# Performance work log

Hardware: AMD Instinct MI355X
Metric: run time of the kernel (lower is better)

The kernel has to match this reference:

```python
import jax, jax.numpy as jnp
import numpy as np

N_EMBD = 768
N_HEADS = 12
HEAD_DIM = N_EMBD // N_HEADS


def _layernorm(x):
    # LayerNorm without affine params, eps=1e-5 (torch default)
    mu = jnp.mean(x, axis=-1, keepdims=True)
    var = jnp.var(x, axis=-1, keepdims=True)
    return (x - mu) * jax.lax.rsqrt(var + 1e-5)


def setup_inputs() -> dict:
    key = jax.random.key(0)
    ks = jax.random.split(key, 6)
    B, T, C = 1, 4096, N_EMBD
    s = lambda fan_in: 1.0 / np.sqrt(fan_in)
    return {
        "x": jax.random.normal(ks[0], (B, T, C), jnp.float32),
        "W_kqv": jax.random.normal(ks[1], (C, 3 * C), jnp.float32) * s(C),
        "W_proj": jax.random.normal(ks[2], (C, C), jnp.float32) * s(C),
        "W_fc": jax.random.normal(ks[3], (C, 2 * C), jnp.float32) * s(C),
        "b_fc": jax.random.normal(ks[4], (2 * C,), jnp.float32) * s(C),
        "W_cproj": jax.random.normal(ks[5], (2 * C, C), jnp.float32) * s(2 * C),
    }


def _attention(h, W_kqv, W_proj):
    B, T, C = h.shape
    kqv = h @ W_kqv                       # (B, T, 3C)
    kqv = kqv.reshape(B, T, 3, N_HEADS, HEAD_DIM)
    k = kqv[:, :, 0]                      # (B, T, H, Dh) -- note k first, per source
    q = kqv[:, :, 1]
    v = kqv[:, :, 2]
    scale = HEAD_DIM ** -0.5
    scores = jnp.einsum('bqhd,bkhd->bhqk', q, k) * scale
    attn = jax.nn.softmax(scores, axis=-1)
    out = jnp.einsum('bhqk,bkhd->bqhd', attn, v).reshape(B, T, C)
    return out @ W_proj


def _mlp(h, W_fc, b_fc, W_cproj):
    h = h @ W_fc + b_fc
    h = jax.nn.gelu(h, approximate=False)  # torch nn.GELU default = exact erf
    return h @ W_cproj


def reference(x, W_kqv, W_proj, W_fc, b_fc, W_cproj):
    x = x + _attention(_layernorm(x), W_kqv, W_proj)
    x = x + _mlp(_layernorm(x), W_fc, b_fc, W_cproj)
    return x
```

## Files before the change

### kernel.cpp

```cpp
#include <hip/hip_runtime.h>
#include <hip/hip_bf16.h>
#include <math.h>

#define T_SEQ 4096
#define C_EMB 768
#define NHEAD 12
#define HDIM  64
#define NZ    4

typedef __bf16 bf16;
typedef __bf16 bf16x8 __attribute__((ext_vector_type(8)));
typedef __bf16 bf16x4 __attribute__((ext_vector_type(4)));
typedef float  f32x4  __attribute__((ext_vector_type(4)));
typedef float  f32x16 __attribute__((ext_vector_type(16)));


__device__ __forceinline__ void stage16(const void* g, void* ldsbase) {
  __builtin_amdgcn_global_load_lds(
      (__attribute__((address_space(1))) const unsigned int*)g,
      (__attribute__((address_space(3))) unsigned int*)ldsbase, 16, 0, 0);
}

__device__ __forceinline__ f32x16 zero16() {
  f32x16 z;
#pragma unroll
  for (int i = 0; i < 16; i++) z[i] = 0.f;
  return z;
}

__global__ void wt_transpose(const float* __restrict__ W, bf16* __restrict__ Wt,
                             int K, int N) {
  __shared__ float tile[32][33];
  const int n0 = blockIdx.x * 32, k0 = blockIdx.y * 32;
  const int tx = threadIdx.x & 31, ty = threadIdx.x >> 5;
#pragma unroll
  for (int i = 0; i < 32; i += 8)
    tile[ty + i][tx] = W[(size_t)(k0 + ty + i) * N + n0 + tx];
  __syncthreads();
#pragma unroll
  for (int i = 0; i < 32; i += 8)
    Wt[(size_t)(n0 + ty + i) * K + k0 + tx] = (bf16)tile[tx][ty + i];
}

__global__ void ln_rows(const float* __restrict__ x, bf16* __restrict__ y) {
  const int row = blockIdx.x;
  const float* xr = x + (size_t)row * C_EMB;
  const int t = threadIdx.x;
  float v0 = xr[t], v1 = xr[t + 256], v2 = xr[t + 512];
  float s  = v0 + v1 + v2;
  float ss = v0 * v0 + v1 * v1 + v2 * v2;
#pragma unroll
  for (int m = 1; m < 64; m <<= 1) {
    s += __shfl_xor(s, m);
    ss += __shfl_xor(ss, m);
  }
  __shared__ float bs[4], bq[4];
  const int w = t >> 6;
  if ((t & 63) == 0) { bs[w] = s; bq[w] = ss; }
  __syncthreads();
  s  = bs[0] + bs[1] + bs[2] + bs[3];
  ss = bq[0] + bq[1] + bq[2] + bq[3];
  const float mu  = s * (1.0f / C_EMB);
  const float var = ss * (1.0f / C_EMB) - mu * mu;
  const float rs  = rsqrtf(var + 1e-5f);
  bf16* yr = y + (size_t)row * C_EMB;
  yr[t]       = (bf16)((v0 - mu) * rs);
  yr[t + 256] = (bf16)((v1 - mu) * rs);
  yr[t + 512] = (bf16)((v2 - mu) * rs);
}

template <int EPI, int BN>
__global__ void gemm_bt(const bf16* __restrict__ A, const bf16* __restrict__ BT,
                        void* __restrict__ Cout, const float* __restrict__ res,
                        const float* __restrict__ bias, int M, int N, int K) {
  __shared__ __align__(16) bf16 As[128 * 64];
  __shared__ __align__(16) bf16 Bs[BN * 64];
  const int row0 = blockIdx.x * 128, col0 = blockIdx.y * BN;
  const int tid = threadIdx.x;
  const int w = tid >> 6, lane = tid & 63;
  const int wr = w >> 1, wc = w & 1;
  const int l15 = lane & 15, l4 = lane >> 4;
  constexpr int NF = BN / 32;

  f32x4 acc[4][NF];
#pragma unroll
  for (int m = 0; m < 4; m++)
#pragma unroll
    for (int n = 0; n < NF; n++) acc[m][n] = (f32x4){0.f, 0.f, 0.f, 0.f};

  const int rr = lane >> 3;
  const int c8 = (lane & 7) * 8;

  for (int k0 = 0; k0 < K; k0 += 64) {
    const bf16* gA = A + (size_t)(row0 + w * 32 + rr) * K + k0 + c8;
    const bf16* gB = BT + (size_t)(col0 + w * (BN / 4) + rr) * K + k0 + c8;
#pragma unroll
    for (int i = 0; i < 4; i++)
      stage16(gA + (size_t)(8 * i) * K, As + (w * 32 + 8 * i) * 64);
#pragma unroll
    for (int i = 0; i < BN / 32; i++)
      stage16(gB + (size_t)(8 * i) * K, Bs + (w * (BN / 4) + 8 * i) * 64);
    __syncthreads();

#pragma unroll
    for (int hh = 0; hh < 2; hh++) {
      bf16x8 af[4], bfv[NF];
#pragma unroll
      for (int m = 0; m < 4; m++)
        af[m] = *reinterpret_cast<const bf16x8*>(
            As + (wr * 64 + m * 16 + l15) * 64 + hh * 32 + l4 * 8);
#pragma unroll
      for (int n = 0; n < NF; n++)
        bfv[n] = *reinterpret_cast<const bf16x8*>(
            Bs + (wc * (BN / 2) + n * 16 + l15) * 64 + hh * 32 + l4 * 8);
#pragma unroll
      for (int m = 0; m < 4; m++)
#pragma unroll
        for (int n = 0; n < NF; n++)
          acc[m][n] = __builtin_amdgcn_mfma_f32_16x16x32_bf16(af[m], bfv[n], acc[m][n], 0, 0, 0);
    }
    __syncthreads();
  }

  const int orow = row0 + wr * 64;
  const int ocol = col0 + wc * (BN / 2);
#pragma unroll
  for (int m = 0; m < 4; m++) {
#pragma unroll
    for (int n = 0; n < NF; n++) {
      const int c = ocol + n * 16 + l15;
#pragma unroll
      for (int j = 0; j < 4; j++) {
        const int r = orow + m * 16 + l4 * 4 + j;
        const size_t idx = (size_t)r * N + c;
        const float v = acc[m][n][j];
        if (EPI == 0) {
          ((bf16*)Cout)[idx] = (bf16)v;
        } else if (EPI == 1) {
          ((float*)Cout)[idx] = res[idx] + v;
        } else if (EPI == 2) {
          const float h = v + bias[c];
          ((bf16*)Cout)[idx] = (bf16)(0.5f * h * (1.0f + erff(h * 0.70710678118f)));
        } else {
          ((float*)Cout)[idx] = res[idx] + v;
        }
      }
    }
  }
}

__global__ __launch_bounds__(256, 3)
void attn_fused(const bf16* __restrict__ kqv,
                bf16* __restrict__ Opart,
                float* __restrict__ Lpart) {
  const int qb = blockIdx.x, h = blockIdx.y, z = blockIdx.z;
  const int tid = threadIdx.x, w = tid >> 6, lane = tid & 63;
  const int l31 = lane & 31, hi = lane >> 5;

  __shared__ __align__(16) char KsB[128 * 144];
  __shared__ __align__(16) char VtB[64 * 272];

  const int qrow = qb * 128 + w * 32 + l31;
  const bf16* qp = kqv + (size_t)qrow * 2304 + 768 + h * 64;
  bf16x8 qf[4];
#pragma unroll
  for (int m = 0; m < 4; m++)
    qf[m] = *reinterpret_cast<const bf16x8*>(qp + hi * 8 + 16 * m);
  const float cscale = 0.125f * 1.4426950408889634f;
#pragma unroll
  for (int m = 0; m < 4; m++)
#pragma unroll
    for (int e = 0; e < 8; e++) qf[m][e] = (bf16)((float)qf[m][e] * cscale);

  bf16x8 ones;
#pragma unroll
  for (int e = 0; e < 8; e++) ones[e] = (bf16)1.0f;

  f32x16 accO0 = zero16(), accO1 = zero16(), accL = zero16();

  const int krow = tid >> 1;
  const int kc0 = (tid & 1) * 4;
  const int kb = tid & 31, db = tid >> 5;
  const int lb = ((kb >> 3) & 3) * 32 + ((kb >> 2) & 1) * 16 + (kb & 1) * 8 +
                 ((kb >> 1) & 1) * 4;

  const int kt0 = z * 8;

  bf16x8 kreg[4], vreg[4];
#define LOADKV(kt)                                                               \
  {                                                                              \
    const bf16* kp =                                                             \
        kqv + (size_t)((kt)*128 + krow) * 2304 + h * 64 + kc0 * 8;               \
    _Pragma("unroll") for (int i = 0; i < 4; i++)                                \
        kreg[i] = *reinterpret_cast<const bf16x8*>(kp + i * 8);                  \
    const bf16* vp =                                                             \
        kqv + (size_t)((kt)*128 + kb * 4) * 2304 + 1536 + h * 64 + db * 8;       \
    _Pragma("unroll") for (int r = 0; r < 4; r++)                                \
        vreg[r] = *reinterpret_cast<const bf16x8*>(vp + (size_t)r * 2304);       \
  }

  LOADKV(kt0);

  for (int kt = 0; kt < 8; kt++) {
    __syncthreads();
    {
      char* kdst = KsB + krow * 144;
#pragma unroll
      for (int i = 0; i < 4; i++)
        *reinterpret_cast<bf16x8*>(kdst + (kc0 + i) * 16) = kreg[i];
#pragma unroll
      for (int e = 0; e < 8; e++) {
        const int d = db * 8 + e;
        const bf16x4 pk4 = (bf16x4){vreg[0][e], vreg[1][e], vreg[2][e], vreg[3][e]};
        *reinterpret_cast<bf16x4*>(VtB + d * 272 + lb * 2) = pk4;
      }
    }
    __syncthreads();
    if (kt + 1 < 8) LOADKV(kt0 + kt + 1);

    bf16x8 pb[8];
#pragma unroll
    for (int t = 0; t < 4; t++) {
      f32x16 st = zero16();
#pragma unroll
      for (int m = 0; m < 4; m++) {
        const bf16x8 kf = *reinterpret_cast<const bf16x8*>(
            KsB + (size_t)(32 * t + l31) * 144 + (2 * m + hi) * 16);
        st = __builtin_amdgcn_mfma_f32_32x32x16_bf16(kf, qf[m], st, 0, 0, 0);
      }
#pragma unroll
      for (int reg = 0; reg < 16; reg++) {
        const float pv = exp2f(st[reg]);
        pb[2 * t + (reg >> 3)][(reg & 3) + 4 * ((reg >> 2) & 1)] = (bf16)pv;
      }
    }

#pragma unroll
    for (int mk = 0; mk < 8; mk++) {
      const bf16x8 vf0 = *reinterpret_cast<const bf16x8*>(
          VtB + (size_t)l31 * 272 + (2 * mk + hi) * 16);
      accO0 = __builtin_amdgcn_mfma_f32_32x32x16_bf16(vf0, pb[mk], accO0, 0, 0, 0);
      const bf16x8 vf1 = *reinterpret_cast<const bf16x8*>(
          VtB + (size_t)(32 + l31) * 272 + (2 * mk + hi) * 16);
      accO1 = __builtin_amdgcn_mfma_f32_32x32x16_bf16(vf1, pb[mk], accO1, 0, 0, 0);
      accL = __builtin_amdgcn_mfma_f32_32x32x16_bf16(ones, pb[mk], accL, 0, 0, 0);
    }
  }
#undef LOADKV

  bf16* Oq = Opart + (size_t)z * T_SEQ * C_EMB + (size_t)qrow * C_EMB + h * 64;
#pragma unroll
  for (int s4 = 0; s4 < 4; s4++) {
    const bf16x4 o0 = (bf16x4){(bf16)accO0[4 * s4 + 0], (bf16)accO0[4 * s4 + 1],
                               (bf16)accO0[4 * s4 + 2], (bf16)accO0[4 * s4 + 3]};
    *reinterpret_cast<bf16x4*>(Oq + 8 * s4 + 4 * hi) = o0;
    const bf16x4 o1 = (bf16x4){(bf16)accO1[4 * s4 + 0], (bf16)accO1[4 * s4 + 1],
                               (bf16)accO1[4 * s4 + 2], (bf16)accO1[4 * s4 + 3]};
    *reinterpret_cast<bf16x4*>(Oq + 32 + 8 * s4 + 4 * hi) = o1;
  }
  if (hi == 0)
    Lpart[(size_t)z * NHEAD * T_SEQ + (size_t)h * T_SEQ + qrow] = accL[0];
}

__global__ void attn_combine(const bf16* __restrict__ Opart,
                             const float* __restrict__ Lpart,
                             bf16* __restrict__ out) {
  const int q = blockIdx.x, t = threadIdx.x;
#pragma unroll
  for (int i = 0; i < 3; i++) {
    const int c = t + i * 256;
    const int h = c >> 6;
    float L = 0.f, O = 0.f;
#pragma unroll
    for (int z = 0; z < NZ; z++) {
      L += Lpart[(size_t)z * NHEAD * T_SEQ + (size_t)h * T_SEQ + q];
      O += (float)Opart[(size_t)z * T_SEQ * C_EMB + (size_t)q * C_EMB + c];
    }
    out[(size_t)q * C_EMB + c] = (bf16)(O / L);
  }
}

extern "C" void kernel_launch(void* const* d_in, const int* in_sizes, int n_in,
                              void* d_out, int out_size, void* d_ws, size_t ws_size,
                              hipStream_t stream) {
  const float* x       = (const float*)d_in[0];
  const float* W_kqv   = (const float*)d_in[1];
  const float* W_proj  = (const float*)d_in[2];
  const float* W_fc    = (const float*)d_in[3];
  const float* b_fc    = (const float*)d_in[4];
  const float* W_cproj = (const float*)d_in[5];
  float* outp = (float*)d_out;

  char* p = (char*)d_ws;
  bf16* Wkqv_t  = (bf16*)p; p += (size_t)2304 * 768 * 2;
  bf16* Wproj_t = (bf16*)p; p += (size_t)768 * 768 * 2;
  bf16* Wfc_t   = (bf16*)p; p += (size_t)1536 * 768 * 2;
  bf16* Wcp_t   = (bf16*)p; p += (size_t)768 * 1536 * 2;
  bf16* A1      = (bf16*)p; p += (size_t)4096 * 768 * 2;
  bf16* KQV     = (bf16*)p; p += (size_t)4096 * 2304 * 2;
  float* x1     = (float*)p; p += (size_t)4096 * 768 * 4;
  bf16* Opart   = (bf16*)p; p += (size_t)NZ * 4096 * 768 * 2;
  float* Lpart  = (float*)p; p += (size_t)NZ * NHEAD * 4096 * 4;
  bf16* attn_o = A1;
  bf16* A2     = KQV;
  bf16* Hg     = KQV + (size_t)4096 * 768;

  wt_transpose<<<dim3(2304 / 32, 768 / 32), 256, 0, stream>>>(W_kqv, Wkqv_t, 768, 2304);
  wt_transpose<<<dim3(768 / 32, 768 / 32), 256, 0, stream>>>(W_proj, Wproj_t, 768, 768);
  wt_transpose<<<dim3(1536 / 32, 768 / 32), 256, 0, stream>>>(W_fc, Wfc_t, 768, 1536);
  wt_transpose<<<dim3(768 / 32, 1536 / 32), 256, 0, stream>>>(W_cproj, Wcp_t, 1536, 768);

  ln_rows<<<4096, 256, 0, stream>>>(x, A1);
  gemm_bt<0, 128><<<dim3(32, 18), 256, 0, stream>>>(A1, Wkqv_t, KQV, nullptr, nullptr,
                                                    4096, 2304, 768);
  attn_fused<<<dim3(32, 12, NZ), 256, 0, stream>>>(KQV, Opart, Lpart);
  attn_combine<<<4096, 256, 0, stream>>>(Opart, Lpart, attn_o);
  gemm_bt<1, 64><<<dim3(32, 12), 256, 0, stream>>>(attn_o, Wproj_t, x1, x, nullptr,
                                                   4096, 768, 768);
  ln_rows<<<4096, 256, 0, stream>>>(x1, A2);
  gemm_bt<2, 64><<<dim3(32, 24), 256, 0, stream>>>(A2, Wfc_t, Hg, nullptr, b_fc,
                                                   4096, 1536, 768);
  gemm_bt<3, 64><<<dim3(32, 12), 256, 0, stream>>>(Hg, Wcp_t, outp, x1, nullptr,
                                                   4096, 768, 1536);
}
```

Baseline: 212.8 us.

## Fuse weight transposes and first layernorm into one prep kernel; remap attention grid

Combines the four weight-transpose launches and the first layernorm into a single prep kernel that dispatches on block index, cutting launch overhead and the idle tails between small kernels. The QKV GEMM moves from BN=128 to BN=64 to get more blocks. The attention grid is flattened to 1D with a swizzled mapping from block to (q-block, head, split), probably aimed at XCD/L2 locality. The softmax exp switches to the hardware exp2 builtin with a vectorized pack. The exp builtin may lose a little accuracy, and the smaller GEMM tile lowers data reuse per block.

```diff
diff --git a/kernel.cpp b/kernel.cpp
--- a/kernel.cpp
+++ b/kernel.cpp
@@ -14,6 +14,12 @@
 typedef float  f32x4  __attribute__((ext_vector_type(4)));
 typedef float  f32x16 __attribute__((ext_vector_type(16)));
 
+#if __has_builtin(__builtin_amdgcn_exp2f)
+#define EXP2 __builtin_amdgcn_exp2f
+#else
+#define EXP2 exp2f
+#endif
+
 
 __device__ __forceinline__ void stage16(const void* g, void* ldsbase) {
   __builtin_amdgcn_global_load_lds(
@@ -28,11 +34,12 @@
   return z;
 }
 
-__global__ void wt_transpose(const float* __restrict__ W, bf16* __restrict__ Wt,
-                             int K, int N) {
-  __shared__ float tile[32][33];
-  const int n0 = blockIdx.x * 32, k0 = blockIdx.y * 32;
-  const int tx = threadIdx.x & 31, ty = threadIdx.x >> 5;
+__device__ __forceinline__ void do_transpose(const float* __restrict__ W,
+                                             bf16* __restrict__ Wt, int K, int N,
+                                             int bx, int by, int tid,
+                                             float (*tile)[33]) {
+  const int n0 = bx * 32, k0 = by * 32;
+  const int tx = tid & 31, ty = tid >> 5;
 #pragma unroll
   for (int i = 0; i < 32; i += 8)
     tile[ty + i][tx] = W[(size_t)(k0 + ty + i) * N + n0 + tx];
@@ -42,10 +49,10 @@
     Wt[(size_t)(n0 + ty + i) * K + k0 + tx] = (bf16)tile[tx][ty + i];
 }
 
-__global__ void ln_rows(const float* __restrict__ x, bf16* __restrict__ y) {
-  const int row = blockIdx.x;
+__device__ __forceinline__ void do_ln(const float* __restrict__ x,
+                                      bf16* __restrict__ y, int row, int t,
+                                      float* red) {
   const float* xr = x + (size_t)row * C_EMB;
-  const int t = threadIdx.x;
   float v0 = xr[t], v1 = xr[t + 256], v2 = xr[t + 512];
   float s  = v0 + v1 + v2;
   float ss = v0 * v0 + v1 * v1 + v2 * v2;
@@ -54,12 +61,11 @@
     s += __shfl_xor(s, m);
     ss += __shfl_xor(ss, m);
   }
-  __shared__ float bs[4], bq[4];
   const int w = t >> 6;
-  if ((t & 63) == 0) { bs[w] = s; bq[w] = ss; }
+  if ((t & 63) == 0) { red[w] = s; red[4 + w] = ss; }
   __syncthreads();
-  s  = bs[0] + bs[1] + bs[2] + bs[3];
-  ss = bq[0] + bq[1] + bq[2] + bq[3];
+  s  = red[0] + red[1] + red[2] + red[3];
+  ss = red[4] + red[5] + red[6] + red[7];
   const float mu  = s * (1.0f / C_EMB);
   const float var = ss * (1.0f / C_EMB) - mu * mu;
   const float rs  = rsqrtf(var + 1e-5f);
@@ -67,6 +73,34 @@
   yr[t]       = (bf16)((v0 - mu) * rs);
   yr[t + 256] = (bf16)((v1 - mu) * rs);
   yr[t + 512] = (bf16)((v2 - mu) * rs);
+}
+
+__global__ void prep(const float* __restrict__ x, bf16* __restrict__ ln_out,
+                     const float* __restrict__ W_kqv, bf16* __restrict__ Wkqv_t,
+                     const float* __restrict__ W_proj, bf16* __restrict__ Wproj_t,
+                     const float* __restrict__ W_fc, bf16* __restrict__ Wfc_t,
+                     const float* __restrict__ W_cproj, bf16* __restrict__ Wcp_t) {
+  __shared__ float tile[32][33];
+  const int b = blockIdx.x, t = threadIdx.x;
+  if (b < 1728) {
+    do_transpose(W_kqv, Wkqv_t, 768, 2304, b % 72, b / 72, t, tile);
+  } else if (b < 2304) {
+    const int bb = b - 1728;
+    do_transpose(W_proj, Wproj_t, 768, 768, bb % 24, bb / 24, t, tile);
+  } else if (b < 3456) {
+    const int bb = b - 2304;
+    do_transpose(W_fc, Wfc_t, 768, 1536, bb % 48, bb / 48, t, tile);
+  } else if (b < 4608) {
+    const int bb = b - 3456;
+    do_transpose(W_cproj, Wcp_t, 1536, 768, bb % 24, bb / 24, t, tile);
+  } else {
+    do_ln(x, ln_out, b - 4608, t, &tile[0][0]);
+  }
+}
+
+__global__ void ln_rows(const float* __restrict__ x, bf16* __restrict__ y) {
+  __shared__ float red[8];
+  do_ln(x, y, blockIdx.x, threadIdx.x, red);
 }
 
 template <int EPI, int BN>
@@ -153,7 +187,11 @@
 void attn_fused(const bf16* __restrict__ kqv,
                 bf16* __restrict__ Opart,
                 float* __restrict__ Lpart) {
-  const int qb = blockIdx.x, h = blockIdx.y, z = blockIdx.z;
+  const int fid = blockIdx.x;
+  const int xs = fid & 7, r = fid >> 3;
+  const int qb = r & 31;
+  const int s = xs * 6 + (r >> 5);
+  const int h = s % 12, z = s / 12;
   const int tid = threadIdx.x, w = tid >> 6, lane = tid & 63;
   const int l31 = lane & 31, hi = lane >> 5;
 
@@ -195,8 +233,8 @@
         kreg[i] = *reinterpret_cast<const bf16x8*>(kp + i * 8);                  \
     const bf16* vp =                                                             \
         kqv + (size_t)((kt)*128 + kb * 4) * 2304 + 1536 + h * 64 + db * 8;       \
-    _Pragma("unroll") for (int r = 0; r < 4; r++)                                \
-        vreg[r] = *reinterpret_cast<const bf16x8*>(vp + (size_t)r * 2304);       \
+    _Pragma("unroll") for (int r2 = 0; r2 < 4; r2++)                             \
+        vreg[r2] = *reinterpret_cast<const bf16x8*>(vp + (size_t)r2 * 2304);     \
   }
 
   LOADKV(kt0);
@@ -229,9 +267,11 @@
         st = __builtin_amdgcn_mfma_f32_32x32x16_bf16(kf, qf[m], st, 0, 0, 0);
       }
 #pragma unroll
-      for (int reg = 0; reg < 16; reg++) {
-        const float pv = exp2f(st[reg]);
-        pb[2 * t + (reg >> 3)][(reg & 3) + 4 * ((reg >> 2) & 1)] = (bf16)pv;
+      for (int hf = 0; hf < 2; hf++) {
+        bf16x8 p;
+#pragma unroll
+        for (int j = 0; j < 8; j++) p[j] = (bf16)EXP2(st[hf * 8 + j]);
+        pb[2 * t + hf] = p;
       }
     }
 
@@ -305,15 +345,11 @@
   bf16* A2     = KQV;
   bf16* Hg     = KQV + (size_t)4096 * 768;
 
-  wt_transpose<<<dim3(2304 / 32, 768 / 32), 256, 0, stream>>>(W_kqv, Wkqv_t, 768, 2304);
-  wt_transpose<<<dim3(768 / 32, 768 / 32), 256, 0, stream>>>(W_proj, Wproj_t, 768, 768);
-  wt_transpose<<<dim3(1536 / 32, 768 / 32), 256, 0, stream>>>(W_fc, Wfc_t, 768, 1536);
-  wt_transpose<<<dim3(768 / 32, 1536 / 32), 256, 0, stream>>>(W_cproj, Wcp_t, 1536, 768);
-
-  ln_rows<<<4096, 256, 0, stream>>>(x, A1);
-  gemm_bt<0, 128><<<dim3(32, 18), 256, 0, stream>>>(A1, Wkqv_t, KQV, nullptr, nullptr,
-                                                    4096, 2304, 768);
-  attn_fused<<<dim3(32, 12, NZ), 256, 0, stream>>>(KQV, Opart, Lpart);
+  prep<<<8704, 256, 0, stream>>>(x, A1, W_kqv, Wkqv_t, W_proj, Wproj_t,
+                                 W_fc, Wfc_t, W_cproj, Wcp_t);
+  gemm_bt<0, 64><<<dim3(32, 36), 256, 0, stream>>>(A1, Wkqv_t, KQV, nullptr, nullptr,
+                                                   4096, 2304, 768);
+  attn_fused<<<1536, 256, 0, stream>>>(KQV, Opart, Lpart);
   attn_combine<<<4096, 256, 0, stream>>>(Opart, Lpart, attn_o);
   gemm_bt<1, 64><<<dim3(32, 12), 256, 0, stream>>>(attn_o, Wproj_t, x1, x, nullptr,
                                                    4096, 768, 768);
```

New measurement: 194.1 us. 1.1x faster.
